# Optimization experiments

Measured on AMD Instinct MI355X. Metric: run time of the kernel, lower is better.

The kernel has to match this reference:

```python
import jax, jax.numpy as jnp
import numpy as np

N_POST = 50000   # dense_shape[0], number of postsynaptic neurons
N_IN = 17400     # dense_shape[1], number of input (LGN) units
NNZ = 1000000    # number of synapses
N_SYN_BASIS = 5  # receptor basis functions
N_SYN_TYPES = 10


def setup_inputs() -> dict:
    key = jax.random.key(0)
    k1, k2, k3, k4, k5, k6 = jax.random.split(key, 6)
    inp = jax.random.normal(k1, (1, 64, N_IN), dtype=jnp.float32)
    rows = jax.random.randint(k2, (NNZ,), 0, N_POST)
    cols = jax.random.randint(k3, (NNZ,), 0, N_IN)
    indices = jnp.stack([rows, cols], axis=1).astype(jnp.int64)  # [nnz, 2]
    input_weights = jax.random.normal(k4, (NNZ,), dtype=jnp.float32)
    synaptic_weights = jax.random.uniform(k5, (N_SYN_TYPES, N_SYN_BASIS), dtype=jnp.float32)
    syn_ids = jax.random.randint(k6, (NNZ,), 0, N_SYN_TYPES).astype(jnp.int64)
    return {"inp": inp, "indices": indices, "input_weights": input_weights,
            "synaptic_weights": synaptic_weights, "syn_ids": syn_ids}


def reference(inp, indices, input_weights, synaptic_weights, syn_ids):
    B, T, n_in = inp.shape
    tokens = B * T
    x = inp.reshape(tokens, n_in)              # flatten (batch, time)
    rows = indices[:, 0]
    cols = indices[:, 1]
    # per-synapse receptor factors: synaptic_weights[syn_ids] -> [nnz, n_basis]
    factors = jnp.take(synaptic_weights, syn_ids, axis=0)
    # gather presynaptic activity once for all receptor bases: [nnz, tokens]
    g = jnp.take(x.T, cols, axis=0)
    outs = []
    for r in range(N_SYN_BASIS):
        vals = input_weights * factors[:, r]                      # [nnz]
        contrib = g * vals[:, None]                               # [nnz, tokens]
        # sparse-dense matmul == segment-sum over destination rows
        out_r = jax.ops.segment_sum(contrib, rows, num_segments=N_POST)  # [n_post, tokens]
        outs.append(out_r)
    i_in = jnp.stack(outs, axis=0)                                # [n_basis, n_post, tokens]
    # tf.transpose of 3D reverses dims -> [tokens, n_post, n_basis]
    out = jnp.transpose(i_in, (2, 1, 0)).reshape(B, T, N_POST * N_SYN_BASIS)
    return out
```

## Files before the change

kernel.cpp:

```cpp
#include <hip/hip_runtime.h>
#include <hip/hip_fp16.h>

#define N_POST 50000
#define N_IN   17400
#define NNZ_E  1000000
#define T_DIM  64
#define R_DIM  5
#define NT_DIM 10

#define BROWS  128
#define NBUCK  ((N_POST + BROWS - 1) / BROWS)
#define EPB    4096
#define NBLK1  ((NNZ_E + EPB - 1) / EPB)
#define CAP    48
#define FCAP   3072
#define CAPR   4608
#define CTILES ((N_IN + 63) / 64)
#define RECBUF_N 1024

static __device__ __forceinline__ unsigned pack2h(float a, float b) {
    __half2 h = __floats2half2_rn(a, b);
    return *reinterpret_cast<unsigned*>(&h);
}

__global__ __launch_bounds__(1024) void k_ts(const float* __restrict__ x,
                                             __half* __restrict__ xT,
                                             const int2* __restrict__ idx2,
                                             const float* __restrict__ iw,
                                             const int* __restrict__ sid,
                                             unsigned short* __restrict__ cnt,
                                             uint2* __restrict__ rec1) {
    __shared__ float tile[64][65];
    int bb = blockIdx.x;
    int tid = threadIdx.x;
    if (bb < CTILES) {
        int c0 = bb * 64;
        int l = tid & 63, w = tid >> 6;
        #pragma unroll
        for (int i = 0; i < 4; ++i) {
            int t = i * 16 + w;
            int c = c0 + l;
            tile[l][t] = (c < N_IN) ? x[t * N_IN + c] : 0.f;
        }
        __syncthreads();
        #pragma unroll
        for (int i = 0; i < 4; ++i) {
            int cc = i * 16 + w;
            int c = c0 + cc;
            if (c < N_IN) xT[c * 64 + l] = __float2half(tile[cc][l]);
        }
        return;
    }
    int* lcur = (int*)&tile[0][0];
    for (int i = tid; i < NBUCK; i += 1024) lcur[i] = 0;
    __syncthreads();
    int blk = bb - CTILES;
    int base = blk * EPB;
    int n = min(EPB, NNZ_E - base);
    for (int i = tid; i < n; i += 1024) {
        int2 rc = idx2[base + i];
        unsigned bk = (unsigned)rc.x >> 7;
        int pos = atomicAdd(&lcur[bk], 1);
        unsigned xx = (unsigned)rc.y | ((unsigned)sid[base + i] << 15)
                    | ((unsigned)(rc.x & 127) << 19);
        rec1[((size_t)bk * NBLK1 + blk) * CAP + pos] =
            make_uint2(xx, __float_as_uint(iw[base + i]));
    }
    __syncthreads();
    for (int i = tid; i < NBUCK; i += 1024)
        cnt[i * NBLK1 + blk] = (unsigned short)lcur[i];
}

__global__ __launch_bounds__(512) void k_fine(const uint2* __restrict__ rec1,
                                              const unsigned short* __restrict__ cnt,
                                              const float* __restrict__ S,
                                              uint4* __restrict__ rec,
                                              int* __restrict__ rstart,
                                              int* __restrict__ plen) {
    __shared__ uint2 lrec[FCAP];
    __shared__ int scnt[256];
    __shared__ int soff[256];
    __shared__ int lhist[BROWS];
    __shared__ int lsc[BROWS];
    __shared__ int lcur[BROWS];
    __shared__ int vp4[BROWS];
    __shared__ float s_S[NT_DIM * R_DIM];
    int t = threadIdx.x;
    int b = blockIdx.x;
    int pbase = b * CAPR;
    if (t < NT_DIM * R_DIM) s_S[t] = S[t];
    int cv = 0;
    if (t < 256) {
        cv = (t < NBLK1) ? (int)cnt[b * NBLK1 + t] : 0;
        scnt[t] = cv;
        soff[t] = cv;
    }
    if (t < BROWS) lhist[t] = 0;
    __syncthreads();
    for (int off = 1; off < 256; off <<= 1) {
        int u = 0;
        if (t < 256 && t >= off) u = soff[t - off];
        __syncthreads();
        if (t < 256) soff[t] += u;
        __syncthreads();
    }
    if (t < 256) soff[t] -= cv;
    __syncthreads();
    const uint2* srcb = rec1 + (size_t)b * NBLK1 * CAP;
    for (int idx = t; idx < NBLK1 * CAP; idx += 512) {
        int cell = idx / CAP;
        int j = idx - cell * CAP;
        if (j < scnt[cell]) lrec[soff[cell] + j] = srcb[idx];
    }
    int nrec = soff[255] + scnt[255];
    __syncthreads();
    for (int i = t; i < nrec; i += 512)
        atomicAdd(&lhist[(lrec[i].x >> 19) & 127], 1);
    __syncthreads();
    if (t < BROWS) vp4[t] = (lhist[t] + 3) & ~3;
    __syncthreads();
    int v = 0, vp = 0;
    if (t < BROWS) {
        v = lhist[t];
        int b4 = t & ~3;
        vp = max(max(vp4[b4], vp4[b4 + 1]), max(vp4[b4 + 2], vp4[b4 + 3]));
        lsc[t] = vp;
    }
    __syncthreads();
    for (int off = 1; off < BROWS; off <<= 1) {
        int u = 0;
        if (t < BROWS && t >= off) u = lsc[t - off];
        __syncthreads();
        if (t < BROWS) lsc[t] += u;
        __syncthreads();
    }
    if (t < BROWS) {
        int exclp = lsc[t] - vp;
        int p = b * BROWS + t;
        if (p < N_POST) { rstart[p] = pbase + exclp; plen[p] = vp; }
        lcur[t] = exclp;
    }
    __syncthreads();
    for (int i = t; i < nrec; i += 512) {
        uint2 rc = lrec[i];
        int r = (rc.x >> 19) & 127;
        int pos = atomicAdd(&lcur[r], 1);
        unsigned col = rc.x & 0x7FFF;
        const float* f = &s_S[((rc.x >> 15) & 0xF) * R_DIM];
        float w = __uint_as_float(rc.y);
        uint4 r4;
        r4.x = col << 7;
        r4.y = pack2h(w * f[0], w * f[1]);
        r4.z = pack2h(w * f[2], w * f[3]);
        r4.w = pack2h(w * f[4], 0.f);
        rec[pbase + pos] = r4;
    }
    if (t < BROWS) {
        int exclp = lsc[t] - vp;
        for (int u = v; u < vp; ++u)
            rec[pbase + exclp + u] = make_uint4(0, 0, 0, 0);
    }
}

#define FMX(acc, xs, xsel, ws, wsel)                                               \
    asm("v_fma_mix_f32 %0, %1, %2, %0 op_sel:[" #xsel "," #wsel ",0] "             \
        "op_sel_hi:[1,1,0]" : "+v"(acc) : "v"(xs), "v"(ws))

#define FMAREC20B(Rk, Xk)                                                          \
    do {                                                                           \
        unsigned xlo_ = (Xk).x, xhi_ = (Xk).y;                                     \
        unsigned w01_ = (Rk).y, w23_ = (Rk).z, w4_ = (Rk).w;                       \
        FMX(a00, xlo_, 0, w01_, 0); FMX(a01, xlo_, 0, w01_, 1);                    \
        FMX(a02, xlo_, 0, w23_, 0); FMX(a03, xlo_, 0, w23_, 1);                    \
        FMX(a04, xlo_, 0, w4_,  0);                                               \
        FMX(a10, xlo_, 1, w01_, 0); FMX(a11, xlo_, 1, w01_, 1);                    \
        FMX(a12, xlo_, 1, w23_, 0); FMX(a13, xlo_, 1, w23_, 1);                    \
        FMX(a14, xlo_, 1, w4_,  0);                                               \
        FMX(a20, xhi_, 0, w01_, 0); FMX(a21, xhi_, 0, w01_, 1);                    \
        FMX(a22, xhi_, 0, w23_, 0); FMX(a23, xhi_, 0, w23_, 1);                    \
        FMX(a24, xhi_, 0, w4_,  0);                                               \
        FMX(a30, xhi_, 1, w01_, 0); FMX(a31, xhi_, 1, w01_, 1);                    \
        FMX(a32, xhi_, 1, w23_, 0); FMX(a33, xhi_, 1, w23_, 1);                    \
        FMX(a34, xhi_, 1, w4_,  0);                                               \
    } while (0)

#define LOADSET4(P0, P1, P2, P3, XX0, XX1, XX2, XX3, q_)                           \
    do {                                                                           \
        P0 = (q_)[0]; P1 = (q_)[1]; P2 = (q_)[2]; P3 = (q_)[3];                    \
        XX0 = *(const uint2*)(xb + (P0.x + s8));                                   \
        XX1 = *(const uint2*)(xb + (P1.x + s8));                                   \
        XX2 = *(const uint2*)(xb + (P2.x + s8));                                   \
        XX3 = *(const uint2*)(xb + (P3.x + s8));                                   \
    } while (0)

#define ROWBODY4(RP)                                                               \
    do {                                                                           \
        if (ng > 0) {                                                              \
            LOADSET4(A0, A1, A2, A3, XA0, XA1, XA2, XA3, (RP));                    \
            int g = 1;                                                             \
            for (; g + 2 <= ng; g += 2) {                                          \
                LOADSET4(B0, B1, B2, B3, XB0, XB1, XB2, XB3, (RP) + (g << 2));     \
                FMAREC20B(A0, XA0); FMAREC20B(A1, XA1);                            \
                FMAREC20B(A2, XA2); FMAREC20B(A3, XA3);                            \
                LOADSET4(A0, A1, A2, A3, XA0, XA1, XA2, XA3,                       \
                         (RP) + ((g + 1) << 2));                                   \
                FMAREC20B(B0, XB0); FMAREC20B(B1, XB1);                            \
                FMAREC20B(B2, XB2); FMAREC20B(B3, XB3);                            \
            }                                                                      \
            if (g < ng) {                                                          \
                LOADSET4(B0, B1, B2, B3, XB0, XB1, XB2, XB3, (RP) + (g << 2));     \
                FMAREC20B(A0, XA0); FMAREC20B(A1, XA1);                            \
                FMAREC20B(A2, XA2); FMAREC20B(A3, XA3);                            \
                FMAREC20B(B0, XB0); FMAREC20B(B1, XB1);                            \
                FMAREC20B(B2, XB2); FMAREC20B(B3, XB3);                            \
            } else {                                                               \
                FMAREC20B(A0, XA0); FMAREC20B(A1, XA1);                            \
                FMAREC20B(A2, XA2); FMAREC20B(A3, XA3);                            \
            }                                                                      \
        }                                                                          \
    } while (0)

__global__ __launch_bounds__(256, 4) void k_phase2(
        const __half* __restrict__ xT, const int* __restrict__ rstart,
        const int* __restrict__ plen, const uint4* __restrict__ rec,
        float* __restrict__ out) {
    __shared__ float o_lds[T_DIM * 81];
    __shared__ uint4 recbuf[RECBUF_N];
    const char* xb = (const char*)xT;
    int tid = threadIdx.x;
    int wave = tid >> 6, lane = tid & 63;
    int q = lane >> 4, s = lane & 15;
    int s8 = s * 8;
    int p0 = blockIdx.x * 16;
    int start0 = rstart[p0];
    int nblk = rstart[p0 + 15] + plen[p0 + 15] - start0;
    bool uselds = (nblk <= RECBUF_N);
    if (uselds) {
        for (int i = tid; i < nblk; i += 256) recbuf[i] = rec[start0 + i];
    }
    __syncthreads();
    int pa = p0 + wave * 4;
    int myrow = pa + q;
    int ih = rstart[myrow];
    int ng = __builtin_amdgcn_readfirstlane(plen[pa]) >> 2;
    float a00 = 0.f, a01 = 0.f, a02 = 0.f, a03 = 0.f, a04 = 0.f;
    float a10 = 0.f, a11 = 0.f, a12 = 0.f, a13 = 0.f, a14 = 0.f;
    float a20 = 0.f, a21 = 0.f, a22 = 0.f, a23 = 0.f, a24 = 0.f;
    float a30 = 0.f, a31 = 0.f, a32 = 0.f, a33 = 0.f, a34 = 0.f;
    uint4 A0, A1, A2, A3, B0, B1, B2, B3;
    uint2 XA0, XA1, XA2, XA3, XB0, XB1, XB2, XB3;
    if (uselds) {
        const uint4* rp = recbuf + (ih - start0);
        ROWBODY4(rp);
    } else {
        const uint4* rp = rec + ih;
        ROWBODY4(rp);
    }
    int rowl = wave * 4 + q;
    {
        float* d0 = &o_lds[(4 * s + 0) * 81 + rowl * 5];
        d0[0] = a00; d0[1] = a01; d0[2] = a02; d0[3] = a03; d0[4] = a04;
        float* d1 = &o_lds[(4 * s + 1) * 81 + rowl * 5];
        d1[0] = a10; d1[1] = a11; d1[2] = a12; d1[3] = a13; d1[4] = a14;
        float* d2 = &o_lds[(4 * s + 2) * 81 + rowl * 5];
        d2[0] = a20; d2[1] = a21; d2[2] = a22; d2[3] = a23; d2[4] = a24;
        float* d3 = &o_lds[(4 * s + 3) * 81 + rowl * 5];
        d3[0] = a30; d3[1] = a31; d3[2] = a32; d3[3] = a33; d3[4] = a34;
    }
    __syncthreads();
    int base5 = blockIdx.x * 80;
    for (int i2 = tid; i2 < T_DIM * 80; i2 += 256) {
        int t = i2 / 80;
        int j = i2 - t * 80;
        out[(size_t)t * (N_POST * R_DIM) + base5 + j] = o_lds[t * 81 + j];
    }
}

extern "C" void kernel_launch(void* const* d_in, const int* in_sizes, int n_in,
                              void* d_out, int out_size, void* d_ws, size_t ws_size,
                              hipStream_t stream) {
    const float* inp  = (const float*)d_in[0];
    const int2*  idx2 = (const int2*)d_in[1];
    const float* iw   = (const float*)d_in[2];
    const float* S    = (const float*)d_in[3];
    const int*   sid  = (const int*)d_in[4];
    float* out = (float*)d_out;

    char* ws = (char*)d_ws;
    size_t off = 0;
    auto alloc = [&](size_t bytes) -> void* {
        void* p = ws + off;
        off += (bytes + 255) & ~(size_t)255;
        return p;
    };
    __half* xT            = (__half*)alloc((size_t)N_IN * T_DIM * 2);
    unsigned short* cnt   = (unsigned short*)alloc((size_t)NBUCK * NBLK1 * 2);
    int*   rstart         = (int*)alloc((size_t)N_POST * 4);
    int*   plen           = (int*)alloc((size_t)N_POST * 4);
    uint2* rec1           = (uint2*)alloc((size_t)NBUCK * NBLK1 * CAP * 8);
    uint4* rec            = (uint4*)alloc((size_t)NBUCK * CAPR * 16);

    k_ts<<<CTILES + NBLK1, 1024, 0, stream>>>(inp, xT, idx2, iw, sid, cnt, rec1);
    k_fine<<<NBUCK, 512, 0, stream>>>(rec1, cnt, S, rec, rstart, plen);
    k_phase2<<<N_POST / 16, 256, 0, stream>>>(xT, rstart, plen, rec, out);
}
```

Measured before the change: 64.28 us.

## Fuse fine bucketing and SpMM phase into one kernel with LDS-resident records

Merges the fine per-row bucketing kernel and the gather/FMA kernel into a single kernel. Each block now owns 64 postsynaptic rows, so the bucket size and capacities shrink, and it builds its padded per-row record list directly in LDS. It then processes the rows in four passes of 16. This removes the global write and readback of the expanded uint4 record array, the rstart/plen arrays and one kernel launch. In exchange it uses more LDS per block (launch bounds drop to 2 blocks per CU), and the fixed capacities (32 records per cell, 2304 LDS records per block) could overflow on denser buckets.

```diff
diff --git a/kernel.cpp b/kernel.cpp
--- a/kernel.cpp
+++ b/kernel.cpp
@@ -8,15 +8,14 @@
 #define R_DIM  5
 #define NT_DIM 10
 
-#define BROWS  128
+#define BROWS  64
 #define NBUCK  ((N_POST + BROWS - 1) / BROWS)
 #define EPB    4096
 #define NBLK1  ((NNZ_E + EPB - 1) / EPB)
-#define CAP    48
-#define FCAP   3072
-#define CAPR   4608
+#define CAP    32
+#define FCAP   1664
+#define FREC   2304
 #define CTILES ((N_IN + 63) / 64)
-#define RECBUF_N 1024
 
 static __device__ __forceinline__ unsigned pack2h(float a, float b) {
     __half2 h = __floats2half2_rn(a, b);
@@ -59,107 +58,16 @@
     int n = min(EPB, NNZ_E - base);
     for (int i = tid; i < n; i += 1024) {
         int2 rc = idx2[base + i];
-        unsigned bk = (unsigned)rc.x >> 7;
+        unsigned bk = (unsigned)rc.x >> 6;
         int pos = atomicAdd(&lcur[bk], 1);
         unsigned xx = (unsigned)rc.y | ((unsigned)sid[base + i] << 15)
-                    | ((unsigned)(rc.x & 127) << 19);
+                    | ((unsigned)(rc.x & 63) << 19);
         rec1[((size_t)bk * NBLK1 + blk) * CAP + pos] =
             make_uint2(xx, __float_as_uint(iw[base + i]));
     }
     __syncthreads();
     for (int i = tid; i < NBUCK; i += 1024)
         cnt[i * NBLK1 + blk] = (unsigned short)lcur[i];
-}
-
-__global__ __launch_bounds__(512) void k_fine(const uint2* __restrict__ rec1,
-                                              const unsigned short* __restrict__ cnt,
-                                              const float* __restrict__ S,
-                                              uint4* __restrict__ rec,
-                                              int* __restrict__ rstart,
-                                              int* __restrict__ plen) {
-    __shared__ uint2 lrec[FCAP];
-    __shared__ int scnt[256];
-    __shared__ int soff[256];
-    __shared__ int lhist[BROWS];
-    __shared__ int lsc[BROWS];
-    __shared__ int lcur[BROWS];
-    __shared__ int vp4[BROWS];
-    __shared__ float s_S[NT_DIM * R_DIM];
-    int t = threadIdx.x;
-    int b = blockIdx.x;
-    int pbase = b * CAPR;
-    if (t < NT_DIM * R_DIM) s_S[t] = S[t];
-    int cv = 0;
-    if (t < 256) {
-        cv = (t < NBLK1) ? (int)cnt[b * NBLK1 + t] : 0;
-        scnt[t] = cv;
-        soff[t] = cv;
-    }
-    if (t < BROWS) lhist[t] = 0;
-    __syncthreads();
-    for (int off = 1; off < 256; off <<= 1) {
-        int u = 0;
-        if (t < 256 && t >= off) u = soff[t - off];
-        __syncthreads();
-        if (t < 256) soff[t] += u;
-        __syncthreads();
-    }
-    if (t < 256) soff[t] -= cv;
-    __syncthreads();
-    const uint2* srcb = rec1 + (size_t)b * NBLK1 * CAP;
-    for (int idx = t; idx < NBLK1 * CAP; idx += 512) {
-        int cell = idx / CAP;
-        int j = idx - cell * CAP;
-        if (j < scnt[cell]) lrec[soff[cell] + j] = srcb[idx];
-    }
-    int nrec = soff[255] + scnt[255];
-    __syncthreads();
-    for (int i = t; i < nrec; i += 512)
-        atomicAdd(&lhist[(lrec[i].x >> 19) & 127], 1);
-    __syncthreads();
-    if (t < BROWS) vp4[t] = (lhist[t] + 3) & ~3;
-    __syncthreads();
-    int v = 0, vp = 0;
-    if (t < BROWS) {
-        v = lhist[t];
-        int b4 = t & ~3;
-        vp = max(max(vp4[b4], vp4[b4 + 1]), max(vp4[b4 + 2], vp4[b4 + 3]));
-        lsc[t] = vp;
-    }
-    __syncthreads();
-    for (int off = 1; off < BROWS; off <<= 1) {
-        int u = 0;
-        if (t < BROWS && t >= off) u = lsc[t - off];
-        __syncthreads();
-        if (t < BROWS) lsc[t] += u;
-        __syncthreads();
-    }
-    if (t < BROWS) {
-        int exclp = lsc[t] - vp;
-        int p = b * BROWS + t;
-        if (p < N_POST) { rstart[p] = pbase + exclp; plen[p] = vp; }
-        lcur[t] = exclp;
-    }
-    __syncthreads();
-    for (int i = t; i < nrec; i += 512) {
-        uint2 rc = lrec[i];
-        int r = (rc.x >> 19) & 127;
-        int pos = atomicAdd(&lcur[r], 1);
-        unsigned col = rc.x & 0x7FFF;
-        const float* f = &s_S[((rc.x >> 15) & 0xF) * R_DIM];
-        float w = __uint_as_float(rc.y);
-        uint4 r4;
-        r4.x = col << 7;
-        r4.y = pack2h(w * f[0], w * f[1]);
-        r4.z = pack2h(w * f[2], w * f[3]);
-        r4.w = pack2h(w * f[4], 0.f);
-        rec[pbase + pos] = r4;
-    }
-    if (t < BROWS) {
-        int exclp = lsc[t] - vp;
-        for (int u = v; u < vp; ++u)
-            rec[pbase + exclp + u] = make_uint4(0, 0, 0, 0);
-    }
 }
 
 #define FMX(acc, xs, xsel, ws, wsel)                                               \
@@ -220,59 +128,131 @@
         }                                                                          \
     } while (0)
 
-__global__ __launch_bounds__(256, 4) void k_phase2(
-        const __half* __restrict__ xT, const int* __restrict__ rstart,
-        const int* __restrict__ plen, const uint4* __restrict__ rec,
-        float* __restrict__ out) {
-    __shared__ float o_lds[T_DIM * 81];
-    __shared__ uint4 recbuf[RECBUF_N];
-    const char* xb = (const char*)xT;
-    int tid = threadIdx.x;
-    int wave = tid >> 6, lane = tid & 63;
+__global__ __launch_bounds__(256, 2) void k_fp(const uint2* __restrict__ rec1,
+                                               const unsigned short* __restrict__ cnt,
+                                               const float* __restrict__ S,
+                                               const __half* __restrict__ xT,
+                                               float* __restrict__ out) {
+    __shared__ uint4 frec[FREC];
+    __shared__ __align__(16) char ubuf[T_DIM * 81 * 4];
+    __shared__ int scnt[256];
+    __shared__ int soff[256];
+    __shared__ int lhist[BROWS];
+    __shared__ int lsc[BROWS];
+    __shared__ int lcur[BROWS];
+    __shared__ int rowst[BROWS];
+    __shared__ int rowlen[BROWS];
+    __shared__ float s_S[NT_DIM * R_DIM];
+    uint2* lrec = (uint2*)ubuf;
+    float* o_lds = (float*)ubuf;
+    int t = threadIdx.x;
+    int b = blockIdx.x;
+    if (t < NT_DIM * R_DIM) s_S[t] = S[t];
+    int cv = (t < NBLK1) ? (int)cnt[b * NBLK1 + t] : 0;
+    scnt[t] = cv;
+    soff[t] = cv;
+    if (t < BROWS) lhist[t] = 0;
+    __syncthreads();
+    for (int off = 1; off < 256; off <<= 1) {
+        int u = (t >= off) ? soff[t - off] : 0;
+        __syncthreads();
+        soff[t] += u;
+        __syncthreads();
+    }
+    soff[t] -= cv;
+    __syncthreads();
+    const uint2* srcb = rec1 + (size_t)b * NBLK1 * CAP;
+    for (int idx = t; idx < NBLK1 * CAP; idx += 256) {
+        int cell = idx >> 5;
+        int j = idx & 31;
+        if (j < scnt[cell]) lrec[soff[cell] + j] = srcb[idx];
+    }
+    int nrec = soff[255] + scnt[255];
+    __syncthreads();
+    for (int i = t; i < nrec; i += 256)
+        atomicAdd(&lhist[(lrec[i].x >> 19) & 63], 1);
+    __syncthreads();
+    if (t < BROWS) rowlen[t] = (lhist[t] + 3) & ~3;
+    __syncthreads();
+    int v = 0, vp = 0;
+    if (t < BROWS) {
+        v = lhist[t];
+        int b4 = t & ~3;
+        vp = max(max(rowlen[b4], rowlen[b4 + 1]), max(rowlen[b4 + 2], rowlen[b4 + 3]));
+        lsc[t] = vp;
+    }
+    __syncthreads();
+    for (int off = 1; off < BROWS; off <<= 1) {
+        int u = 0;
+        if (t < BROWS && t >= off) u = lsc[t - off];
+        __syncthreads();
+        if (t < BROWS) lsc[t] += u;
+        __syncthreads();
+    }
+    if (t < BROWS) {
+        int excl = lsc[t] - vp;
+        rowst[t] = excl;
+        rowlen[t] = vp;
+        lcur[t] = excl;
+    }
+    __syncthreads();
+    for (int i = t; i < nrec; i += 256) {
+        uint2 rc = lrec[i];
+        int r = (rc.x >> 19) & 63;
+        int pos = atomicAdd(&lcur[r], 1);
+        unsigned col = rc.x & 0x7FFF;
+        const float* f = &s_S[((rc.x >> 15) & 0xF) * R_DIM];
+        float w = __uint_as_float(rc.y);
+        uint4 r4;
+        r4.x = col << 7;
+        r4.y = pack2h(w * f[0], w * f[1]);
+        r4.z = pack2h(w * f[2], w * f[3]);
+        r4.w = pack2h(w * f[4], 0.f);
+        frec[pos] = r4;
+    }
+    if (t < BROWS) {
+        for (int u2 = v; u2 < vp; ++u2)
+            frec[rowst[t] + u2] = make_uint4(0, 0, 0, 0);
+    }
+    __syncthreads();
+    int wave = t >> 6, lane = t & 63;
     int q = lane >> 4, s = lane & 15;
     int s8 = s * 8;
-    int p0 = blockIdx.x * 16;
-    int start0 = rstart[p0];
-    int nblk = rstart[p0 + 15] + plen[p0 + 15] - start0;
-    bool uselds = (nblk <= RECBUF_N);
-    if (uselds) {
-        for (int i = tid; i < nblk; i += 256) recbuf[i] = rec[start0 + i];
-    }
-    __syncthreads();
-    int pa = p0 + wave * 4;
-    int myrow = pa + q;
-    int ih = rstart[myrow];
-    int ng = __builtin_amdgcn_readfirstlane(plen[pa]) >> 2;
-    float a00 = 0.f, a01 = 0.f, a02 = 0.f, a03 = 0.f, a04 = 0.f;
-    float a10 = 0.f, a11 = 0.f, a12 = 0.f, a13 = 0.f, a14 = 0.f;
-    float a20 = 0.f, a21 = 0.f, a22 = 0.f, a23 = 0.f, a24 = 0.f;
-    float a30 = 0.f, a31 = 0.f, a32 = 0.f, a33 = 0.f, a34 = 0.f;
-    uint4 A0, A1, A2, A3, B0, B1, B2, B3;
-    uint2 XA0, XA1, XA2, XA3, XB0, XB1, XB2, XB3;
-    if (uselds) {
-        const uint4* rp = recbuf + (ih - start0);
+    const char* xb = (const char*)xT;
+    #pragma unroll 1
+    for (int pass = 0; pass < 4; ++pass) {
+        int rloc = pass * 16 + wave * 4 + q;
+        int ng = __builtin_amdgcn_readfirstlane(rowlen[pass * 16 + wave * 4]) >> 2;
+        int ih = rowst[rloc];
+        float a00 = 0.f, a01 = 0.f, a02 = 0.f, a03 = 0.f, a04 = 0.f;
+        float a10 = 0.f, a11 = 0.f, a12 = 0.f, a13 = 0.f, a14 = 0.f;
+        float a20 = 0.f, a21 = 0.f, a22 = 0.f, a23 = 0.f, a24 = 0.f;
+        float a30 = 0.f, a31 = 0.f, a32 = 0.f, a33 = 0.f, a34 = 0.f;
+        uint4 A0, A1, A2, A3, B0, B1, B2, B3;
+        uint2 XA0, XA1, XA2, XA3, XB0, XB1, XB2, XB3;
+        const uint4* rp = frec + ih;
         ROWBODY4(rp);
-    } else {
-        const uint4* rp = rec + ih;
-        ROWBODY4(rp);
-    }
-    int rowl = wave * 4 + q;
-    {
-        float* d0 = &o_lds[(4 * s + 0) * 81 + rowl * 5];
-        d0[0] = a00; d0[1] = a01; d0[2] = a02; d0[3] = a03; d0[4] = a04;
-        float* d1 = &o_lds[(4 * s + 1) * 81 + rowl * 5];
-        d1[0] = a10; d1[1] = a11; d1[2] = a12; d1[3] = a13; d1[4] = a14;
-        float* d2 = &o_lds[(4 * s + 2) * 81 + rowl * 5];
-        d2[0] = a20; d2[1] = a21; d2[2] = a22; d2[3] = a23; d2[4] = a24;
-        float* d3 = &o_lds[(4 * s + 3) * 81 + rowl * 5];
-        d3[0] = a30; d3[1] = a31; d3[2] = a32; d3[3] = a33; d3[4] = a34;
-    }
-    __syncthreads();
-    int base5 = blockIdx.x * 80;
-    for (int i2 = tid; i2 < T_DIM * 80; i2 += 256) {
-        int t = i2 / 80;
-        int j = i2 - t * 80;
-        out[(size_t)t * (N_POST * R_DIM) + base5 + j] = o_lds[t * 81 + j];
+        int rowl = wave * 4 + q;
+        {
+            float* d0 = &o_lds[(4 * s + 0) * 81 + rowl * 5];
+            d0[0] = a00; d0[1] = a01; d0[2] = a02; d0[3] = a03; d0[4] = a04;
+            float* d1 = &o_lds[(4 * s + 1) * 81 + rowl * 5];
+            d1[0] = a10; d1[1] = a11; d1[2] = a12; d1[3] = a13; d1[4] = a14;
+            float* d2 = &o_lds[(4 * s + 2) * 81 + rowl * 5];
+            d2[0] = a20; d2[1] = a21; d2[2] = a22; d2[3] = a23; d2[4] = a24;
+            float* d3 = &o_lds[(4 * s + 3) * 81 + rowl * 5];
+            d3[0] = a30; d3[1] = a31; d3[2] = a32; d3[3] = a33; d3[4] = a34;
+        }
+        __syncthreads();
+        int base5 = (b * BROWS + pass * 16) * 5;
+        int maxj = N_POST * R_DIM - base5;
+        for (int i2 = t; i2 < T_DIM * 80; i2 += 256) {
+            int tt = i2 / 80;
+            int j = i2 - tt * 80;
+            if (j < maxj)
+                out[(size_t)tt * (N_POST * R_DIM) + base5 + j] = o_lds[tt * 81 + j];
+        }
+        __syncthreads();
     }
 }
 
@@ -295,12 +275,8 @@
     };
     __half* xT            = (__half*)alloc((size_t)N_IN * T_DIM * 2);
     unsigned short* cnt   = (unsigned short*)alloc((size_t)NBUCK * NBLK1 * 2);
-    int*   rstart         = (int*)alloc((size_t)N_POST * 4);
-    int*   plen           = (int*)alloc((size_t)N_POST * 4);
     uint2* rec1           = (uint2*)alloc((size_t)NBUCK * NBLK1 * CAP * 8);
-    uint4* rec            = (uint4*)alloc((size_t)NBUCK * CAPR * 16);
 
     k_ts<<<CTILES + NBLK1, 1024, 0, stream>>>(inp, xT, idx2, iw, sid, cnt, rec1);
-    k_fine<<<NBUCK, 512, 0, stream>>>(rec1, cnt, S, rec, rstart, plen);
-    k_phase2<<<N_POST / 16, 256, 0, stream>>>(xT, rstart, plen, rec, out);
-}
+    k_fp<<<NBUCK, 256, 0, stream>>>(rec1, cnt, S, xT, out);
+}
```

Result: slower. 90.77 us (+41.2%).
